# Optimization experiments

Hardware: AMD Instinct MI355X
Metric: run time of the kernel (lower is better)

## Reference

```python
import math
import jax, jax.numpy as jnp
import numpy as np

B = 2
TMAX = 1024
D = 1024
H = 16
DK = D // H
F = 4096
L = 2
CHUNK = 128
LEFT = 128
RIGHT = 32
EPS = 1e-5


def _build_mask(t_max, chunk, left, right):
    """Replicates EmformerEncoder.create_mask with audio_lens == t_max.
    Returns bool [T, T] where True = masked (disallowed), T = total_right + t_max."""
    num_chunks = math.ceil(t_max / chunk)
    ub = (num_chunks - 1) * right
    body = np.zeros((t_max, t_max), np.float32)
    mleft = np.zeros((t_max, ub), np.float32)
    mdiag = np.zeros((ub, ub), np.float32)
    mright = np.zeros((ub, t_max), np.float32)
    right_indexes = []
    for i in range(num_chunks):
        left_off = max(chunk * i - left, 0)
        start = chunk * i
        end = min(chunk * (i + 1), t_max)
        body[start:end, left_off:end] = 1
        if i == num_chunks - 1:
            break
        rem = t_max - (end + right)
        trl = right if rem >= 0 else t_max - end
        ri = len(right_indexes)
        mleft[start:start + chunk, ri:ri + trl] = 1
        mdiag[ri:ri + trl, ri:ri + trl] = 1
        mright[ri:ri + trl, left_off:end] = 1
        right_indexes += list(range(end, end + trl))
    rs = len(right_indexes)
    mleft = mleft[:, :rs]
    mdiag = mdiag[:rs, :rs]
    mright = mright[:rs, :]
    top = np.concatenate([mdiag, mright], axis=-1)
    bot = np.concatenate([mleft, body], axis=-1)
    m = np.concatenate([top, bot], axis=0)
    return m == 0  # True where attention is NOT allowed


def setup_inputs() -> dict:
    key = jax.random.key(0)
    ks = jax.random.split(key, 8)
    mask2d = _build_mask(TMAX, CHUNK, LEFT, RIGHT)  # [T, T]
    T = mask2d.shape[0]  # 1248
    w = lambda k, shape: jax.random.normal(k, shape, jnp.float32) * 0.02
    inp = {
        "input": jax.random.normal(ks[0], (B, T, D), jnp.float32),
        "ln_in_scale": jnp.ones((L, D), jnp.float32),
        "ln_in_bias": jnp.zeros((L, D), jnp.float32),
        "Wq": w(ks[1], (L, D, D)), "bq": jnp.zeros((L, D), jnp.float32),
        "Wk": w(ks[2], (L, D, D)), "bk": jnp.zeros((L, D), jnp.float32),
        "Wv": w(ks[3], (L, D, D)), "bv": jnp.zeros((L, D), jnp.float32),
        "ln1_scale": jnp.ones((L, D), jnp.float32),
        "ln1_bias": jnp.zeros((L, D), jnp.float32),
        "W1": w(ks[4], (L, D, F)), "b1": jnp.zeros((L, F), jnp.float32),
        "W2": w(ks[5], (L, F, D)), "b2": jnp.zeros((L, D), jnp.float32),
        "ln2_scale": jnp.ones((L, D), jnp.float32),
        "ln2_bias": jnp.zeros((L, D), jnp.float32),
        "mask": jnp.asarray(np.broadcast_to(mask2d[None, None], (B, 1, T, T)).copy()),
    }
    return inp


def _ln(x, scale, bias):
    m = jnp.mean(x, axis=-1, keepdims=True)
    v = jnp.mean(jnp.square(x - m), axis=-1, keepdims=True)
    return (x - m) * jax.lax.rsqrt(v + EPS) * scale + bias


def reference(input, ln_in_scale, ln_in_bias, Wq, bq, Wk, bk, Wv, bv,
              ln1_scale, ln1_bias, W1, b1, W2, b2, ln2_scale, ln2_bias, mask):
    x = input
    Bx, T, _ = x.shape
    scale = 1.0 / math.sqrt(DK)
    for l in range(L):
        h = _ln(x, ln_in_scale[l], ln_in_bias[l])  # pre-LN input (also residual base)
        q = (h @ Wq[l] + bq[l]).reshape(Bx, T, H, DK)
        k = (h @ Wk[l] + bk[l]).reshape(Bx, T, H, DK)
        v = (h @ Wv[l] + bv[l]).reshape(Bx, T, H, DK)
        scores = jnp.einsum('bqhd,bkhd->bhqk', q, k) * scale  # [B,H,T,T]
        scores = jnp.where(mask, -jnp.inf, scores)
        probs = jax.nn.softmax(scores, axis=-1)
        probs = jnp.where(mask, 0.0, probs)  # dropout_attn=0 -> identity
        o = jnp.einsum('bhqk,bkhd->bqhd', probs, v).reshape(Bx, T, D)
        attn_out = o + h
        y = _ln(attn_out, ln1_scale[l], ln1_bias[l])
        y = y @ W1[l] + b1[l]          # note: no activation in original code
        y = y @ W2[l] + b2[l] + attn_out
        x = _ln(y, ln2_scale[l], ln2_bias[l])
    return x
```

## Files before the change

kernel.cpp:

```cpp
#include <hip/hip_runtime.h>
#include <stdint.h>

typedef __attribute__((ext_vector_type(8))) short short8;
typedef __attribute__((ext_vector_type(4))) float f32x4;
typedef __attribute__((ext_vector_type(2))) _Float16 half2_t;

#define DEV __device__ __forceinline__

DEV float bits2f(uint32_t u){ union{uint32_t u;float f;}v; v.u=u; return v.f; }
DEV float bf_lo(uint32_t w){ return bits2f(w<<16); }
DEV float bf_hi(uint32_t w){ return bits2f(w & 0xffff0000u); }
DEV float bf1(uint16_t s){ return bits2f(((uint32_t)s)<<16); }
DEV uint16_t f2bf(float f){ union{float f;uint32_t u;}v; v.f=f; uint32_t u=v.u;
  return (uint16_t)((u + 0x7fffu + ((u>>16)&1u))>>16); }
DEV uint16_t f2h(float a){ union{_Float16 h; uint16_t u;}v; v.h=(_Float16)a; return v.u; }
DEV float h2f(uint16_t s){ union{uint16_t u; _Float16 h;}v; v.u=s; return (float)v.h; }

DEV float ldval(const float* p, size_t i){ return p[i]; }
DEV float ldval(const uint16_t* p, size_t i){ return bf1(p[i]); }
DEV void stval(float* p, size_t i, float v){ p[i]=v; }
DEV void stval(uint16_t* p, size_t i, float v){ p[i]=f2bf(v); }

DEV void async16(const void* g, void* l){
#if __has_builtin(__builtin_amdgcn_global_load_lds)
  __builtin_amdgcn_global_load_lds((const __attribute__((address_space(1))) void*)g,
                                   (__attribute__((address_space(3))) void*)l, 16, 0, 0);
#else
  int lane = threadIdx.x & 63;
  *(uint4*)((char*)l + lane*16) = *(const uint4*)((const char*)g);
#endif
}

template<int TM, int TN, bool SPLIT>
__global__ __launch_bounds__(256) void gemm_t(
    const uint16_t* __restrict__ A, const uint16_t* __restrict__ Bt,
    const float* __restrict__ bias, void* __restrict__ Cout,
    int N, int K, int kchunk) {
  __shared__ uint16_t sA[2][TM*32];
  __shared__ uint16_t sB[2][TN*32];
  const int m0 = blockIdx.y*TM, n0 = blockIdx.x*TN;
  const int kb = SPLIT ? blockIdx.z*kchunk : 0;
  const int kend = SPLIT ? kb + kchunk : K;
  const int tid = threadIdx.x, wid = tid>>6, lane = tid&63;
  constexpr int WM = TM/2, MT = WM/16;
  constexpr int WN = TN/2, NT = WN/16;
  const int wm = (wid&1)*WM, wn = (wid>>1)*WN;
  f32x4 acc[MT][NT];
  #pragma unroll
  for (int a=0;a<MT;a++)
    #pragma unroll
    for (int b=0;b<NT;b++) acc[a][b] = (f32x4){0.f,0.f,0.f,0.f};
  const int lrow = lane>>2, lcol = (lane&3)*8;

  for (int k0 = kb; k0 < kend; k0 += 64) {
    __syncthreads();
    #pragma unroll
    for (int h=0; h<2; ++h) {
      #pragma unroll
      for (int j = 0; j < TM/64; ++j) {
        int r0 = wid*(TM/4) + j*16;
        async16(A + (size_t)(m0+r0+lrow)*K + k0+h*32 + lcol, &sA[h][r0*32]);
      }
      #pragma unroll
      for (int j = 0; j < TN/64; ++j) {
        int r0 = wid*(TN/4) + j*16;
        async16(Bt + (size_t)(n0+r0+lrow)*K + k0+h*32 + lcol, &sB[h][r0*32]);
      }
    }
    __syncthreads();
    #pragma unroll
    for (int h=0; h<2; ++h) {
      short8 af[MT], bfv[NT];
      #pragma unroll
      for (int t=0;t<MT;t++) af[t] = *(const short8*)&sA[h][(wm + t*16 + (lane&15))*32 + (lane>>4)*8];
      #pragma unroll
      for (int t=0;t<NT;t++) bfv[t] = *(const short8*)&sB[h][(wn + t*16 + (lane&15))*32 + (lane>>4)*8];
      #pragma unroll
      for (int mt=0;mt<MT;mt++)
        #pragma unroll
        for (int nt=0;nt<NT;nt++)
          acc[mt][nt] = __builtin_amdgcn_mfma_f32_16x16x32_bf16(af[mt], bfv[nt], acc[mt][nt], 0,0,0);
    }
  }
  const int cl = lane&15, rl = (lane>>4)*4;
  if (SPLIT) {
    float* Pz = (float*)Cout + (size_t)blockIdx.z*2560*N;
    #pragma unroll
    for (int nt=0;nt<NT;nt++) {
      int n = n0 + wn + nt*16 + cl;
      #pragma unroll
      for (int mt=0;mt<MT;mt++)
        #pragma unroll
        for (int r=0;r<4;r++)
          Pz[(size_t)(m0 + wm + mt*16 + rl + r)*N + n] = acc[mt][nt][r];
    }
  } else {
    uint16_t* C = (uint16_t*)Cout;
    #pragma unroll
    for (int nt=0;nt<NT;nt++) {
      int n = n0 + wn + nt*16 + cl;
      float bv = bias ? bias[n] : 0.f;
      #pragma unroll
      for (int mt=0;mt<MT;mt++)
        #pragma unroll
        for (int r=0;r<4;r++)
          C[(size_t)(m0 + wm + mt*16 + rl + r)*N + n] = f2bf(acc[mt][nt][r] + bv);
    }
  }
}

template<typename TI, typename TO>
DEV void ln_body(int row, int tid, const TI* x, const float* sc, const float* bi,
                 TO* out, float* red) {
  const size_t base = (size_t)row*1024 + tid*4;
  float v0=ldval(x,base), v1=ldval(x,base+1), v2=ldval(x,base+2), v3=ldval(x,base+3);
  float s = v0+v1+v2+v3;
  float sq = v0*v0+v1*v1+v2*v2+v3*v3;
  #pragma unroll
  for (int off=32; off; off>>=1){ s += __shfl_xor(s,off); sq += __shfl_xor(sq,off); }
  int wid=tid>>6, lane=tid&63;
  if (lane==0){ red[wid]=s; red[4+wid]=sq; }
  __syncthreads();
  s = red[0]+red[1]+red[2]+red[3]; sq = red[4]+red[5]+red[6]+red[7];
  float mean = s*(1.f/1024.f);
  float inv  = rsqrtf(sq*(1.f/1024.f) - mean*mean + 1e-5f);
  int c = tid*4;
  stval(out, base,   (v0-mean)*inv*sc[c]   + bi[c]);
  stval(out, base+1, (v1-mean)*inv*sc[c+1] + bi[c+1]);
  stval(out, base+2, (v2-mean)*inv*sc[c+2] + bi[c+2]);
  stval(out, base+3, (v3-mean)*inv*sc[c+3] + bi[c+3]);
}

template<typename TI, typename TO>
__global__ __launch_bounds__(256) void ln_k(const TI* __restrict__ x,
    const float* __restrict__ sc, const float* __restrict__ bi,
    TO* __restrict__ out) {
  __shared__ float red[8];
  ln_body<TI,TO>(blockIdx.x, threadIdx.x, x, sc, bi, out, red);
}

template<typename TO>
__global__ __launch_bounds__(256) void ln2_fused(const float* __restrict__ P,
    const float* __restrict__ b2, const uint16_t* __restrict__ resid,
    const float* __restrict__ sc, const float* __restrict__ bi,
    TO* __restrict__ out) {
  const int row = blockIdx.x, tid = threadIdx.x;
  const size_t base = (size_t)row*1024 + tid*4;
  float4 p0 = *(const float4*)(P + base);
  float4 p1 = *(const float4*)(P + (size_t)2560*1024 + base);
  int c = tid*4;
  float v0 = p0.x+p1.x+b2[c]  +bf1(resid[base]);
  float v1 = p0.y+p1.y+b2[c+1]+bf1(resid[base+1]);
  float v2 = p0.z+p1.z+b2[c+2]+bf1(resid[base+2]);
  float v3 = p0.w+p1.w+b2[c+3]+bf1(resid[base+3]);
  float s = v0+v1+v2+v3;
  float sq = v0*v0+v1*v1+v2*v2+v3*v3;
  #pragma unroll
  for (int off=32; off; off>>=1){ s += __shfl_xor(s,off); sq += __shfl_xor(sq,off); }
  __shared__ float red[8];
  int wid=tid>>6, lane=tid&63;
  if (lane==0){ red[wid]=s; red[4+wid]=sq; }
  __syncthreads();
  s = red[0]+red[1]+red[2]+red[3]; sq = red[4]+red[5]+red[6]+red[7];
  float mean = s*(1.f/1024.f);
  float inv  = rsqrtf(sq*(1.f/1024.f) - mean*mean + 1e-5f);
  stval(out, base,   (v0-mean)*inv*sc[c]   + bi[c]);
  stval(out, base+1, (v1-mean)*inv*sc[c+1] + bi[c+1]);
  stval(out, base+2, (v2-mean)*inv*sc[c+2] + bi[c+2]);
  stval(out, base+3, (v3-mean)*inv*sc[c+3] + bi[c+3]);
}

__global__ __launch_bounds__(256) void attn_fused(
    const uint32_t* __restrict__ qkv32, const uint16_t* __restrict__ hres,
    uint16_t* __restrict__ attn_out) {
  const int blk = blockIdx.x;
  const int qg = blk & 3, ci = (blk>>2)&7, hh = (blk>>5)&15, bb = blk>>9;
  const int sum_cnt = (ci<7)?32:0;
  const int bstart = (ci>=1)?128*(ci-1):0;
  const int bend = (ci==7)?1024:128*(ci+1);
  const int nk = sum_cnt + (bend - bstart);
  const int rowbase = bb*1248;
  const int tid = threadIdx.x, wid = tid>>6, lane = tid&63;
  const int fr = lane&15, fc = lane>>4;

  __shared__ uint16_t sm[30848];
  uint16_t* K16 = sm;
  uint32_t* KD  = (uint32_t*)sm;
  uint16_t* Q16 = sm + 20736;
  uint32_t* QD  = KD + 10368;
  uint16_t* SP16 = sm;
  uint16_t* V16 = sm + 11840;
  uint32_t* VD  = (uint32_t*)(sm + 11840);

  for (int idx = tid; idx < nk*32; idx += 256) {
    int j = idx>>5, d2 = idx&31;
    int tk = (j < sum_cnt) ? (32*ci + j) : (224 + bstart + (j - sum_cnt));
    KD[j*36 + d2] = qkv32[(size_t)(rowbase+tk)*1536 + 512 + hh*32 + d2];
  }
  for (int idx = tid; idx < 40*32; idx += 256) {
    int j = idx>>5, d2 = idx&31;
    int ql = qg*40 + j;
    int tq = (ql<32) ? (32*ci+ql) : (224+128*ci+ql-32);
    QD[j*36 + d2] = qkv32[(size_t)(rowbase+tq)*1536 + hh*32 + d2];
  }
  __syncthreads();

  const int n_mt = nk>>4;
  const int qoff[3] = {0,16,24};
  f32x4 accs[5][3];
  #pragma unroll
  for (int a=0;a<5;a++)
    #pragma unroll
    for (int b=0;b<3;b++) accs[a][b] = (f32x4){0.f,0.f,0.f,0.f};
  #pragma unroll
  for (int ks=0; ks<2; ++ks) {
    short8 bq_[3];
    #pragma unroll
    for (int nt=0;nt<3;nt++)
      bq_[nt] = *(const short8*)&Q16[(qoff[nt]+fr)*72 + ks*32 + fc*8];
    #pragma unroll
    for (int t=0;t<5;t++) {
      int mt = wid + 4*t;
      if (mt < n_mt) {
        short8 a_ = *(const short8*)&K16[(mt*16+fr)*72 + ks*32 + fc*8];
        #pragma unroll
        for (int nt=0;nt<3;nt++)
          accs[t][nt] = __builtin_amdgcn_mfma_f32_16x16x32_bf16(a_, bq_[nt], accs[t][nt], 0,0,0);
      }
    }
  }
  __syncthreads();

  #pragma unroll
  for (int t=0;t<5;t++) {
    int mt = wid + 4*t;
    if (mt < n_mt) {
      #pragma unroll
      for (int nt=0;nt<3;nt++) {
        int q = qoff[nt] + fr;
        #pragma unroll
        for (int r=0;r<4;r++)
          SP16[q*296 + mt*16 + fc*4 + r] = f2h(accs[t][nt][r]*0.125f);
      }
    }
  }
  for (int idx = tid; idx < nk*32; idx += 256) {
    int j = idx>>5, d2 = idx&31;
    int tk = (j < sum_cnt) ? (32*ci + j) : (224 + bstart + (j - sum_cnt));
    VD[j*33 + d2] = qkv32[(size_t)(rowbase+tk)*1536 + 1024 + hh*32 + d2];
  }
  __syncthreads();

  for (int i=0;i<10;i++) {
    int row = wid*10 + i;
    float v[5];
    #pragma unroll
    for (int g=0;g<5;g++){ int k=g*64+lane; v[g] = (k<nk) ? h2f(SP16[row*296+k]) : -1e30f; }
    float mx = fmaxf(fmaxf(fmaxf(v[0],v[1]),fmaxf(v[2],v[3])),v[4]);
    #pragma unroll
    for (int off=32; off; off>>=1) mx = fmaxf(mx, __shfl_xor(mx,off));
    float p[5], sum=0.f;
    #pragma unroll
    for (int g=0;g<5;g++){ p[g] = __expf(v[g]-mx); if (g*64+lane>=nk) p[g]=0.f; sum+=p[g]; }
    #pragma unroll
    for (int off=32; off; off>>=1) sum += __shfl_xor(sum,off);
    float inv = 1.f/sum;
    #pragma unroll
    for (int g=0;g<5;g++){ int k=g*64+lane; if (k<nk) SP16[row*296+k] = f2bf(p[g]*inv); }
  }
  __syncthreads();

  const int nkt = nk>>5;
  f32x4 acco[3];
  #pragma unroll
  for (int t=0;t<3;t++) acco[t] = (f32x4){0.f,0.f,0.f,0.f};
  const uint16_t* vcol = V16 + wid*16 + fr;
  for (int kt=0; kt<nkt; ++kt) {
    short8 bv_;
    #pragma unroll
    for (int j=0;j<8;j++) bv_[j] = (short)vcol[(kt*32 + fc*8 + j)*66];
    #pragma unroll
    for (int t=0;t<3;t++) {
      short8 a_ = *(const short8*)&SP16[(qoff[t]+fr)*296 + kt*32 + fc*8];
      acco[t] = __builtin_amdgcn_mfma_f32_16x16x32_bf16(a_, bv_, acco[t], 0,0,0);
    }
  }
  #pragma unroll
  for (int t=0;t<3;t++) {
    #pragma unroll
    for (int r=0;r<4;r++) {
      bool vq = true;
      if (ci==7 && qg==0 && (qoff[t]+fc*4+r)<32) vq = false;
      if (vq) {
        int qll = qg*40 + qoff[t] + fc*4 + r;
        int tq = (qll<32) ? (32*ci+qll) : (224+128*ci+qll-32);
        size_t addr = (size_t)(rowbase+tq)*1024 + hh*64 + wid*16 + fr;
        attn_out[addr] = f2bf(acco[t][r] + bf1(hres[addr]));
      }
    }
  }
}

__global__ void prep_k(const float* __restrict__ Wq, const float* __restrict__ Wk,
                       const float* __restrict__ Wv, const float* __restrict__ W1,
                       const float* __restrict__ W2, const float* __restrict__ bq,
                       const float* __restrict__ bk, const float* __restrict__ bv,
                       uint16_t* __restrict__ wt_qkv, uint16_t* __restrict__ wt_w1,
                       uint16_t* __restrict__ wt_w2, float* __restrict__ bqkv,
                       const void* __restrict__ lnx, int lnx_f32,
                       const float* __restrict__ lnsc, const float* __restrict__ lnbi,
                       uint16_t* __restrict__ lnout) {
  __shared__ float t[32][33];
  const int blk = blockIdx.x;
  const int tx = threadIdx.x, ty = threadIdx.y;
  if (blk >= 11276) {
    int row = blk - 11276;
    int tid = ty*32 + tx;
    float* red = &t[0][0];
    if (lnx_f32) ln_body<float,uint16_t>((int)row, tid, (const float*)lnx, lnsc, lnbi, lnout, red);
    else         ln_body<uint16_t,uint16_t>((int)row, tid, (const uint16_t*)lnx, lnsc, lnbi, lnout, red);
    return;
  }
  if (blk >= 11264) {
    int i = (blk-11264)*256 + ty*32 + tx;
    bqkv[i] = (i<1024) ? bq[i] : ((i<2048) ? bk[i-1024] : bv[i-2048]);
    return;
  }
  const float* src; uint16_t* dst; int R, C, c0, r0;
  if (blk < 3072) {
    int w = blk>>10, tt = blk&1023;
    src = (w==0)?Wq:((w==1)?Wk:Wv); dst = wt_qkv + (size_t)w*1048576;
    R = 1024; C = 1024; c0 = (tt&31)*32; r0 = (tt>>5)*32;
  } else if (blk < 7168) {
    int tt = blk-3072;
    src = W1; dst = wt_w1; R = 1024; C = 4096;
    c0 = (tt&127)*32; r0 = (tt>>7)*32;
  } else {
    int tt = blk-7168;
    src = W2; dst = wt_w2; R = 4096; C = 1024;
    c0 = (tt&31)*32; r0 = (tt>>5)*32;
  }
  #pragma unroll
  for (int i=0;i<4;i++) t[ty+8*i][tx] = src[(size_t)(r0+ty+8*i)*C + c0+tx];
  __syncthreads();
  #pragma unroll
  for (int i=0;i<4;i++) dst[(size_t)(c0+ty+8*i)*R + r0+tx] = f2bf(t[tx][ty+8*i]);
}

extern "C" void kernel_launch(void* const* d_in, const int* in_sizes, int n_in,
                              void* d_out, int out_size, void* d_ws, size_t ws_size,
                              hipStream_t stream) {
  const float* input  = (const float*)d_in[0];
  const float* lnin_s = (const float*)d_in[1];
  const float* lnin_b = (const float*)d_in[2];
  const float* Wq = (const float*)d_in[3];
  const float* bq = (const float*)d_in[4];
  const float* Wk = (const float*)d_in[5];
  const float* bk = (const float*)d_in[6];
  const float* Wv = (const float*)d_in[7];
  const float* bv = (const float*)d_in[8];
  const float* ln1_s = (const float*)d_in[9];
  const float* ln1_b = (const float*)d_in[10];
  const float* W1 = (const float*)d_in[11];
  const float* b1 = (const float*)d_in[12];
  const float* W2 = (const float*)d_in[13];
  const float* b2 = (const float*)d_in[14];
  const float* ln2_s = (const float*)d_in[15];
  const float* ln2_b = (const float*)d_in[16];

  char* ws = (char*)d_ws;
  uint16_t* wt_qkv = (uint16_t*)(ws + 0);
  uint16_t* wt_w1  = (uint16_t*)(ws + 6291456);
  uint16_t* wt_w2  = (uint16_t*)(ws + 14680064);
  float*    bqkv   = (float*)   (ws + 23068672);
  uint16_t* hbuf   = (uint16_t*)(ws + 23080960);
  uint16_t* qkvb   = (uint16_t*)(ws + 28323840);
  uint16_t* attnb  = (uint16_t*)(ws + 44052480);
  uint16_t* zbuf   = (uint16_t*)(ws + 49295360);
  float*    pbuf   = (float*)   (ws + 54538240);
  uint16_t* y1b    = hbuf;
  uint16_t* x1b    = zbuf;

  const uint16_t* xcur_bf = x1b;
  for (int l=0; l<2; ++l) {
    prep_k<<<13772, dim3(32,8), 0, stream>>>(Wq+(size_t)l*1048576, Wk+(size_t)l*1048576,
        Wv+(size_t)l*1048576, W1+(size_t)l*4194304, W2+(size_t)l*4194304,
        bq+l*1024, bk+l*1024, bv+l*1024, wt_qkv, wt_w1, wt_w2, bqkv,
        (l==0) ? (const void*)input : (const void*)xcur_bf, (l==0)?1:0,
        lnin_s+l*1024, lnin_b+l*1024, hbuf);

    gemm_t<128,128,false><<<dim3(24,20),256,0,stream>>>(hbuf, wt_qkv, bqkv, qkvb, 3072, 1024, 1024);
    attn_fused<<<1024,256,0,stream>>>((const uint32_t*)qkvb, hbuf, attnb);
    ln_k<uint16_t,uint16_t><<<2496,256,0,stream>>>(attnb, ln1_s+l*1024, ln1_b+l*1024, zbuf);
    gemm_t<128,128,false><<<dim3(32,20),256,0,stream>>>(zbuf, wt_w1, b1+l*4096, y1b, 4096, 1024, 1024);
    gemm_t<128,128,true><<<dim3(8,20,2),256,0,stream>>>(y1b, wt_w2, nullptr, pbuf, 1024, 4096, 2048);
    if (l==1) ln2_fused<float>   <<<2496,256,0,stream>>>(pbuf, b2+l*1024, attnb, ln2_s+l*1024, ln2_b+l*1024, (float*)d_out);
    else      ln2_fused<uint16_t><<<2496,256,0,stream>>>(pbuf, b2+l*1024, attnb, ln2_s+l*1024, ln2_b+l*1024, x1b);
  }
  (void)in_sizes; (void)n_in; (void)out_size; (void)ws_size;
}
```

Measured before the change: 501.2 us.

## Double-buffer GEMM LDS stages, XOR-swizzle LDS layout, and remap block order

The GEMM main loop becomes a software pipeline over 32-wide K steps. The next K step is loaded asynchronously into the other LDS buffer while the current one is consumed, replacing the old load-then-wait pattern that had two barriers per 64-wide step. The LDS column index is XOR-swizzled on both store and load to reduce bank conflicts on the fragment reads. Tile indices are remapped so that consecutive blocks are spread into eight strided groups, meant to improve L2 reuse. Risks: the block remap assumes the grid size is divisible by 8, and correctness relies on the barrier also waiting for the async LDS loads to finish.

```diff
diff --git a/kernel.cpp b/kernel.cpp
--- a/kernel.cpp
+++ b/kernel.cpp
@@ -38,7 +38,11 @@
     int N, int K, int kchunk) {
   __shared__ uint16_t sA[2][TM*32];
   __shared__ uint16_t sB[2][TN*32];
-  const int m0 = blockIdx.y*TM, n0 = blockIdx.x*TN;
+  const int lin = blockIdx.y*gridDim.x + blockIdx.x;
+  const int q8 = (gridDim.x*gridDim.y) >> 3;
+  const int swz = (lin & 7)*q8 + (lin >> 3);
+  const int mt_ = swz % gridDim.y, nt_ = swz / gridDim.y;
+  const int m0 = mt_*TM, n0 = nt_*TN;
   const int kb = SPLIT ? blockIdx.z*kchunk : 0;
   const int kend = SPLIT ? kb + kchunk : K;
   const int tid = threadIdx.x, wid = tid>>6, lane = tid&63;
@@ -50,37 +54,40 @@
   for (int a=0;a<MT;a++)
     #pragma unroll
     for (int b=0;b<NT;b++) acc[a][b] = (f32x4){0.f,0.f,0.f,0.f};
-  const int lrow = lane>>2, lcol = (lane&3)*8;
-
-  for (int k0 = kb; k0 < kend; k0 += 64) {
+  const int lrow = lane>>2;
+  const int lcol = (((lane&3) ^ ((lrow>>1)&3)))*8;
+  const int fr = lane&15, fc = lane>>4;
+  const int rsw = (fc ^ ((fr>>1)&3))*8;
+
+  auto stage = [&](int buf, int k0) {
+    #pragma unroll
+    for (int j = 0; j < TM/64; ++j) {
+      int r0 = wid*(TM/4) + j*16;
+      async16(A + (size_t)(m0+r0+lrow)*K + k0 + lcol, &sA[buf][r0*32]);
+    }
+    #pragma unroll
+    for (int j = 0; j < TN/64; ++j) {
+      int r0 = wid*(TN/4) + j*16;
+      async16(Bt + (size_t)(n0+r0+lrow)*K + k0 + lcol, &sB[buf][r0*32]);
+    }
+  };
+
+  const int niter = (kend - kb) >> 5;
+  stage(0, kb);
+  for (int it = 0; it < niter; ++it) {
     __syncthreads();
-    #pragma unroll
-    for (int h=0; h<2; ++h) {
+    if (it+1 < niter) stage((it+1)&1, kb + (it+1)*32);
+    const int bsel = it&1;
+    short8 af[MT], bfv[NT];
+    #pragma unroll
+    for (int t=0;t<MT;t++) af[t] = *(const short8*)&sA[bsel][(wm + t*16 + fr)*32 + rsw];
+    #pragma unroll
+    for (int t=0;t<NT;t++) bfv[t] = *(const short8*)&sB[bsel][(wn + t*16 + fr)*32 + rsw];
+    #pragma unroll
+    for (int mt=0;mt<MT;mt++)
       #pragma unroll
-      for (int j = 0; j < TM/64; ++j) {
-        int r0 = wid*(TM/4) + j*16;
-        async16(A + (size_t)(m0+r0+lrow)*K + k0+h*32 + lcol, &sA[h][r0*32]);
-      }
-      #pragma unroll
-      for (int j = 0; j < TN/64; ++j) {
-        int r0 = wid*(TN/4) + j*16;
-        async16(Bt + (size_t)(n0+r0+lrow)*K + k0+h*32 + lcol, &sB[h][r0*32]);
-      }
-    }
-    __syncthreads();
-    #pragma unroll
-    for (int h=0; h<2; ++h) {
-      short8 af[MT], bfv[NT];
-      #pragma unroll
-      for (int t=0;t<MT;t++) af[t] = *(const short8*)&sA[h][(wm + t*16 + (lane&15))*32 + (lane>>4)*8];
-      #pragma unroll
-      for (int t=0;t<NT;t++) bfv[t] = *(const short8*)&sB[h][(wn + t*16 + (lane&15))*32 + (lane>>4)*8];
-      #pragma unroll
-      for (int mt=0;mt<MT;mt++)
-        #pragma unroll
-        for (int nt=0;nt<NT;nt++)
-          acc[mt][nt] = __builtin_amdgcn_mfma_f32_16x16x32_bf16(af[mt], bfv[nt], acc[mt][nt], 0,0,0);
-    }
+      for (int nt=0;nt<NT;nt++)
+        acc[mt][nt] = __builtin_amdgcn_mfma_f32_16x16x32_bf16(af[mt], bfv[nt], acc[mt][nt], 0,0,0);
   }
   const int cl = lane&15, rl = (lane>>4)*4;
   if (SPLIT) {
```

Result: no change. 505.8 us (+0.9%).
